# Kernel tuning notes

Measured on AMD Instinct MI355X. Metric: run time of the kernel, lower is better.

Reference implementation:

```python
import jax, jax.numpy as jnp
import numpy as np

N_NODES = 50000
N_EDGES = 800000
N_GRAPHS = 256


def setup_inputs() -> dict:
    key = jax.random.key(0)
    ks = jax.random.split(key, 20)
    s = 0.05
    return {
        "x": jax.random.normal(ks[0], (N_NODES, 128), jnp.float32),
        "edge_index": jax.random.randint(ks[1], (2, N_EDGES), 0, N_NODES, jnp.int64),
        "batch_index": jnp.sort(jax.random.randint(ks[2], (N_NODES,), 0, N_GRAPHS, jnp.int64)),
        "mol_features": jax.random.normal(ks[3], (N_GRAPHS, 256), jnp.float32),
        "gcn_W": jax.random.normal(ks[4], (3, 128, 128), jnp.float32) * s,
        "gcn_b": jax.random.normal(ks[5], (3, 128), jnp.float32) * s,
        "gcn_out_W": jax.random.normal(ks[6], (128, 128), jnp.float32) * s,
        "gcn_out_b": jax.random.normal(ks[7], (128,), jnp.float32) * s,
        "mlp_W": jax.random.normal(ks[8], (2, 256, 256), jnp.float32) * s,
        "mlp_b": jax.random.normal(ks[9], (2, 256), jnp.float32) * s,
        "mlp_out_W": jax.random.normal(ks[10], (64, 256), jnp.float32) * s,
        "mlp_out_b": jax.random.normal(ks[11], (64,), jnp.float32) * s,
        "pred_W1": jax.random.normal(ks[12], (256, 192), jnp.float32) * s,
        "pred_b1": jax.random.normal(ks[13], (256,), jnp.float32) * s,
        "pred_W2": jax.random.normal(ks[14], (256, 256), jnp.float32) * s,
        "pred_b2": jax.random.normal(ks[15], (256,), jnp.float32) * s,
        "out_W": jax.random.normal(ks[16], (1, 256), jnp.float32) * s,
        "out_b": jax.random.normal(ks[17], (1,), jnp.float32) * s,
    }


def reference(x, edge_index, batch_index, mol_features,
              gcn_W, gcn_b, gcn_out_W, gcn_out_b,
              mlp_W, mlp_b, mlp_out_W, mlp_out_b,
              pred_W1, pred_b1, pred_W2, pred_b2, out_W, out_b):
    N = x.shape[0]
    E = edge_index.shape[1]
    G = mol_features.shape[0]
    row, col = edge_index[0], edge_index[1]

    # GCN normalization with self-loops (PyG gcn_norm, symmetric):
    # deg[i] = in-degree(i) + 1 (self loop); norm_e = d^-1/2[row] * d^-1/2[col]
    deg = jax.ops.segment_sum(jnp.ones((E,), x.dtype), col, num_segments=N) + 1.0
    dinv = jax.lax.rsqrt(deg)
    enorm = (dinv[row] * dinv[col])[:, None]     # [E,1]
    self_c = (dinv * dinv)[:, None]              # [N,1] self-loop coefficient

    h1 = x
    for i in range(gcn_W.shape[0]):
        h = h1 @ gcn_W[i].T                      # per-node transform [N,128]
        agg = jax.ops.segment_sum(h[row] * enorm, col, num_segments=N)
        h1 = jax.nn.relu(agg + self_c * h + gcn_b[i])
    h1 = h1 @ gcn_out_W.T + gcn_out_b            # final GCN-branch Linear (no relu)

    # global_mean_pool over batch_index -> [G,128]
    sums = jax.ops.segment_sum(h1, batch_index, num_segments=G)
    counts = jax.ops.segment_sum(jnp.ones((N,), x.dtype), batch_index, num_segments=G)
    h1 = sums / jnp.maximum(counts, 1.0)[:, None]

    # MLP branch: relu after every linear (including last)
    h2 = mol_features
    for i in range(mlp_W.shape[0]):
        h2 = jax.nn.relu(h2 @ mlp_W[i].T + mlp_b[i])
    h2 = jax.nn.relu(h2 @ mlp_out_W.T + mlp_out_b)

    h = jnp.concatenate([h1, h2], axis=1)        # [G,192]
    h = jax.nn.relu(h @ pred_W1.T + pred_b1)
    h = jax.nn.relu(h @ pred_W2.T + pred_b2)
    return h @ out_W.T + out_b                   # [G,1]
```

## Files before the change

kernel.cpp:

```cpp
#include <hip/hip_runtime.h>


typedef __attribute__((ext_vector_type(8))) short short8;
typedef __attribute__((ext_vector_type(4))) float f32x4;

#define BKT 64
#define SL 16
#define CAP 192
#define WCAP 2560
#define NBINBLK 2048
#define HROWS 65536

__device__ __forceinline__ unsigned short f2bf(float f) {
    union { float f; unsigned u; } c; c.f = f;
    unsigned u = c.u;
    unsigned r = u + 0x7FFFu + ((u >> 16) & 1u);
    return (unsigned short)(r >> 16);
}
__device__ __forceinline__ float bflo(unsigned w) {
    union { unsigned u; float f; } c; c.u = w << 16; return c.f;
}
__device__ __forceinline__ float bfhi(unsigned w) {
    union { unsigned u; float f; } c; c.u = w & 0xFFFF0000u; return c.f;
}

__global__ void k_init(int* cur, float* pool, float* cnt,
                       const float* __restrict__ gcnW, uint4* __restrict__ Wb,
                       int M, int G) {
    int i = blockIdx.x * 256 + threadIdx.x;
    if (i < M * 16) cur[i] = 0;
    if (i < G * 128) pool[i] = 0.f;
    if (i < G) cnt[i] = 0.f;
    if (i < 3 * 2048) {
        int l = i >> 11, rem = i & 2047;
        int o = rem >> 4, c = rem & 15;
        const float4* s = (const float4*)(gcnW + (size_t)l * 16384 + o * 128 + c * 8);
        float4 a = s[0], b = s[1];
        uint4 v;
        v.x = ((unsigned)f2bf(a.y) << 16) | f2bf(a.x);
        v.y = ((unsigned)f2bf(a.w) << 16) | f2bf(a.z);
        v.z = ((unsigned)f2bf(b.y) << 16) | f2bf(b.x);
        v.w = ((unsigned)f2bf(b.w) << 16) | f2bf(b.z);
        Wb[(l << 11) | (o << 4) | (c ^ (o & 15))] = v;
    }
}

__global__ __launch_bounds__(256) void k_bin(const int* __restrict__ row,
                                             const int* __restrict__ col,
                                             int* __restrict__ cur,
                                             unsigned* __restrict__ gbin,
                                             int E, int C) {
    const int x = blockIdx.x & (SL - 1);
    int e0 = blockIdx.x * C, e1 = min(E, e0 + C);
    for (int e = e0 + threadIdx.x; e < e1; e += 256) {
        int c = col[e];
        int cell = (c >> 6) * SL + x;
        int cnt = atomicAdd(&cur[cell << 4], 1);
        gbin[cell * CAP + cnt] = (unsigned)row[e] | ((unsigned)(c & 63) << 16);
    }
}

__global__ __launch_bounds__(256) void k_csr(const unsigned* __restrict__ gbin,
                                             const int* __restrict__ cur,
                                             int* __restrict__ rs,
                                             unsigned short* __restrict__ rd,
                                             float* __restrict__ dinv,
                                             unsigned short* __restrict__ csrf,
                                             const float* __restrict__ x,
                                             unsigned short* __restrict__ xb,
                                             int N) {
    const int b = blockIdx.x, t = threadIdx.x;
    __shared__ int hcnt[64], lcur[64], fills[SL];
    __shared__ float sdinv[64];
    if (t < 64) hcnt[t] = 0;
    if (t < SL) fills[t] = cur[(b * SL + t) << 4];
    __syncthreads();
    #pragma unroll 4
    for (int xx = 0; xx < SL; ++xx) {
        int cbase = (b * SL + xx) * CAP, fill = fills[xx];
        for (int i = t; i < fill; i += 256)
            atomicAdd(&hcnt[(gbin[cbase + i] >> 16) & 63], 1);
    }
    __syncthreads();
    if (t < 64) {
        int v = hcnt[t], xs = v;
        #pragma unroll
        for (int off = 1; off < 64; off <<= 1) {
            int u = __shfl_up(xs, off, 64);
            if (t >= off) xs += u;
        }
        int excl = xs - v;
        lcur[t] = excl;
        float d = rsqrtf((float)v + 1.0f);
        sdinv[t] = d;
        int node = b * 64 + t;
        rs[node] = b * WCAP + excl;
        rd[node] = (unsigned short)v;
        dinv[node] = d;
    }
    __syncthreads();
    #pragma unroll 4
    for (int xx = 0; xx < SL; ++xx) {
        int cbase = (b * SL + xx) * CAP, fill = fills[xx];
        for (int i = t; i < fill; i += 256) {
            unsigned v = gbin[cbase + i];
            int p = atomicAdd(&lcur[(v >> 16) & 63], 1);
            csrf[b * WCAP + p] = (unsigned short)(v & 0xFFFFu);
        }
    }
    const int node0 = b * 64;
    #pragma unroll
    for (int it = 0; it < 4; ++it) {
        int i = t + it * 256;
        int nd = node0 + (i >> 4);
        if (nd < N) {
            int ch = i & 15;
            float d = sdinv[i >> 4];
            const float4* s = (const float4*)(x + (size_t)nd * 128 + ch * 8);
            float4 a = s[0], bb = s[1];
            uint4 o;
            o.x = ((unsigned)f2bf(d * a.y) << 16) | f2bf(d * a.x);
            o.y = ((unsigned)f2bf(d * a.w) << 16) | f2bf(d * a.z);
            o.z = ((unsigned)f2bf(d * bb.y) << 16) | f2bf(d * bb.x);
            o.w = ((unsigned)f2bf(d * bb.w) << 16) | f2bf(d * bb.z);
            *(uint4*)(xb + (size_t)nd * 128 + ch * 8) = o;
        }
    }
}

__global__ __launch_bounds__(256) void k_agg(const unsigned short* __restrict__ h,
                                             unsigned short* __restrict__ y,
                                             const float* __restrict__ dinv,
                                             const int* __restrict__ rs,
                                             const unsigned short* __restrict__ rd,
                                             const unsigned short* __restrict__ csrf,
                                             int N) {
    const int lane = threadIdx.x & 63;
    const int n = blockIdx.x * 4 + (threadIdx.x >> 6);
    if (n >= N) return;
    const int fg = lane & 15;
    const int slot = lane >> 4;
    const int s = rs[n], e = s + rd[n];

    float acc[8] = {0.f, 0.f, 0.f, 0.f, 0.f, 0.f, 0.f, 0.f};
    for (int base = s; base < e; base += 16) {
        int src_l = csrf[base + fg];
        #pragma unroll
        for (int i = 0; i < 4; ++i) {
            int j = i * 4 + slot;
            int src = __shfl(src_l, j, 16);
            uint4 v = *(const uint4*)(h + (size_t)src * 128 + fg * 8);
            bool ok = (base + j) < e;
            v.x = ok ? v.x : 0u; v.y = ok ? v.y : 0u;
            v.z = ok ? v.z : 0u; v.w = ok ? v.w : 0u;
            acc[0] += bflo(v.x); acc[1] += bfhi(v.x);
            acc[2] += bflo(v.y); acc[3] += bfhi(v.y);
            acc[4] += bflo(v.z); acc[5] += bfhi(v.z);
            acc[6] += bflo(v.w); acc[7] += bfhi(v.w);
        }
    }
    #pragma unroll
    for (int r = 0; r < 8; ++r) {
        acc[r] += __shfl_xor(acc[r], 16, 64);
        acc[r] += __shfl_xor(acc[r], 32, 64);
    }
    if (slot == 0) {
        float dn = dinv[n];
        uint4 hv = *(const uint4*)(h + (size_t)n * 128 + fg * 8);
        float sv[8] = {bflo(hv.x), bfhi(hv.x), bflo(hv.y), bfhi(hv.y),
                       bflo(hv.z), bfhi(hv.z), bflo(hv.w), bfhi(hv.w)};
        unsigned short ob[8];
        #pragma unroll
        for (int r = 0; r < 8; ++r) ob[r] = f2bf(dn * (acc[r] + sv[r]));
        uint4 o;
        o.x = ((unsigned)ob[1] << 16) | ob[0];
        o.y = ((unsigned)ob[3] << 16) | ob[2];
        o.z = ((unsigned)ob[5] << 16) | ob[4];
        o.w = ((unsigned)ob[7] << 16) | ob[6];
        *(uint4*)(y + (size_t)n * 128 + fg * 8) = o;
    }
}

__global__ __launch_bounds__(256) void k_mm(const unsigned short* __restrict__ A,
                                            const uint4* __restrict__ Wb,
                                            const float* __restrict__ bias,
                                            const float* __restrict__ dscale,
                                            unsigned short* __restrict__ C, int N) {
    __shared__ uint4 Wsh[2048];
    const int tid = threadIdx.x;
    #pragma unroll
    for (int it = 0; it < 8; ++it)
        Wsh[tid + it * 256] = Wb[tid + it * 256];

    const int lane = tid & 63;
    const int wv = tid >> 6;
    const int l15 = lane & 15, quad = lane >> 4;
    const int arow_i = blockIdx.x * 64 + wv * 16 + l15;
    const unsigned short* arow = A + (size_t)min(arow_i, N - 1) * 128;

    f32x4 acc[8];
    #pragma unroll
    for (int ct = 0; ct < 8; ++ct) acc[ct] = (f32x4){0.f, 0.f, 0.f, 0.f};

    __syncthreads();
    #pragma unroll
    for (int kiter = 0; kiter < 4; ++kiter) {
        short8 af = *(const short8*)(arow + kiter * 32 + quad * 8);
        const int cswz = (kiter * 4 + quad) ^ l15;
        #pragma unroll
        for (int ct = 0; ct < 8; ++ct) {
            short8 bf = *(const short8*)(&Wsh[((ct * 16 + l15) << 4) | cswz]);
            acc[ct] = __builtin_amdgcn_mfma_f32_16x16x32_bf16(af, bf, acc[ct], 0, 0, 0);
        }
    }

    const int rbase = blockIdx.x * 64 + wv * 16 + quad * 4;
    float ds[4];
    #pragma unroll
    for (int r = 0; r < 4; ++r) {
        int rr = rbase + r;
        ds[r] = (dscale && rr < N) ? dscale[rr] : 1.f;
    }
    #pragma unroll
    for (int ct = 0; ct < 8; ++ct) {
        int colc = ct * 16 + l15;
        float bcol = bias[colc];
        #pragma unroll
        for (int r = 0; r < 4; ++r) {
            int rr = rbase + r;
            if (rr < N) {
                float v = fmaxf(acc[ct][r] + bcol, 0.f) * ds[r];
                C[(size_t)rr * 128 + colc] = f2bf(v);
            }
        }
    }
}

__global__ __launch_bounds__(256) void k_pool(const unsigned short* __restrict__ h,
                                              const int* __restrict__ batch,
                                              float* __restrict__ pool,
                                              float* __restrict__ cnt, int N) {
    int t = threadIdx.x;
    int fg = t & 15, sg = t >> 4;
    int n0 = blockIdx.x * 512 + sg * 32;
    if (n0 >= N) return;
    int n1 = min(n0 + 32, N);
    int gprev = batch[n0];
    float racc[8] = {0.f, 0.f, 0.f, 0.f, 0.f, 0.f, 0.f, 0.f};
    float rcnt = 0.f;
    for (int n = n0; n < n1; ++n) {
        int g = batch[n];
        if (g != gprev) {
            float* dst = pool + (size_t)gprev * 128 + fg * 8;
            #pragma unroll
            for (int r = 0; r < 8; ++r) atomicAdd(dst + r, racc[r]);
            if (fg == 0) atomicAdd(&cnt[gprev], rcnt);
            #pragma unroll
            for (int r = 0; r < 8; ++r) racc[r] = 0.f;
            rcnt = 0.f; gprev = g;
        }
        uint4 v = *(const uint4*)(h + (size_t)n * 128 + fg * 8);
        racc[0] += bflo(v.x); racc[1] += bfhi(v.x);
        racc[2] += bflo(v.y); racc[3] += bfhi(v.y);
        racc[4] += bflo(v.z); racc[5] += bfhi(v.z);
        racc[6] += bflo(v.w); racc[7] += bfhi(v.w);
        rcnt += 1.f;
    }
    float* dst = pool + (size_t)gprev * 128 + fg * 8;
    #pragma unroll
    for (int r = 0; r < 8; ++r) atomicAdd(dst + r, racc[r]);
    if (fg == 0) atomicAdd(&cnt[gprev], rcnt);
}

__device__ __forceinline__ float dot8(const float* __restrict__ S,
                                      const float* __restrict__ w, int K32) {
    float a[8] = {0.f, 0.f, 0.f, 0.f, 0.f, 0.f, 0.f, 0.f};
    for (int i = 0; i < K32; ++i) {
        #pragma unroll
        for (int j = 0; j < 8; ++j) {
            float4 wv = *(const float4*)(w + i * 32 + j * 4);
            float4 sv = *(const float4*)(S + i * 32 + j * 4);
            a[j] += wv.x * sv.x + wv.y * sv.y + wv.z * sv.z + wv.w * sv.w;
        }
    }
    return ((a[0] + a[1]) + (a[2] + a[3])) + ((a[4] + a[5]) + (a[6] + a[7]));
}

__global__ __launch_bounds__(256) void k_head(
    const float* __restrict__ pool, const float* __restrict__ cnt,
    const float* __restrict__ gcnoW, const float* __restrict__ gcnob,
    const float* __restrict__ mol,
    const float* __restrict__ mlpW, const float* __restrict__ mlpb,
    const float* __restrict__ mloW, const float* __restrict__ mlob,
    const float* __restrict__ pW1, const float* __restrict__ pb1,
    const float* __restrict__ pW2, const float* __restrict__ pb2,
    const float* __restrict__ oW, const float* __restrict__ ob,
    float* __restrict__ out, int G) {
    const int g = blockIdx.x;
    const int t = threadIdx.x;
    __shared__ float A[256], B[256], Cc[192], Mn[128];
    __shared__ float red[4];

    A[t] = mol[(size_t)g * 256 + t];
    if (t < 128) {
        float c = cnt[g];
        Mn[t] = pool[(size_t)g * 128 + t] / fmaxf(c, 1.f);
    }
    __syncthreads();

    float v = dot8(A, mlpW + (size_t)t * 256, 8);
    B[t] = fmaxf(v + mlpb[t], 0.f);
    __syncthreads();

    v = dot8(B, mlpW + 65536 + (size_t)t * 256, 8);
    A[t] = fmaxf(v + mlpb[256 + t], 0.f);
    __syncthreads();

    if (t < 64) {
        float a2 = dot8(A, mloW + (size_t)t * 256, 8);
        Cc[128 + t] = fmaxf(a2 + mlob[t], 0.f);
    } else if (t < 192) {
        int o = t - 64;
        float a2 = dot8(Mn, gcnoW + (size_t)o * 128, 4);
        Cc[o] = a2 + gcnob[o];
    }
    __syncthreads();

    v = dot8(Cc, pW1 + (size_t)t * 192, 6);
    B[t] = fmaxf(v + pb1[t], 0.f);
    __syncthreads();

    v = dot8(B, pW2 + (size_t)t * 256, 8);
    float r = fmaxf(v + pb2[t], 0.f) * oW[t];
    #pragma unroll
    for (int off = 32; off > 0; off >>= 1) r += __shfl_xor(r, off, 64);
    if ((t & 63) == 0) red[t >> 6] = r;
    __syncthreads();
    if (t == 0) out[g] = red[0] + red[1] + red[2] + red[3] + ob[0];
}

extern "C" void kernel_launch(void* const* d_in, const int* in_sizes, int n_in,
                              void* d_out, int out_size, void* d_ws, size_t ws_size,
                              hipStream_t stream) {
    const float* x     = (const float*)d_in[0];
    const int*   ei    = (const int*)d_in[1];
    const int*   batch = (const int*)d_in[2];
    const float* mol   = (const float*)d_in[3];
    const float* gcnW  = (const float*)d_in[4];
    const float* gcnb  = (const float*)d_in[5];
    const float* gcnoW = (const float*)d_in[6];
    const float* gcnob = (const float*)d_in[7];
    const float* mlpW  = (const float*)d_in[8];
    const float* mlpb  = (const float*)d_in[9];
    const float* mloW  = (const float*)d_in[10];
    const float* mlob  = (const float*)d_in[11];
    const float* pW1   = (const float*)d_in[12];
    const float* pb1   = (const float*)d_in[13];
    const float* pW2   = (const float*)d_in[14];
    const float* pb2   = (const float*)d_in[15];
    const float* oW    = (const float*)d_in[16];
    const float* ob    = (const float*)d_in[17];

    const int N = in_sizes[0] / 128;
    const int E = in_sizes[1] / 2;
    const int G = in_sizes[3] / 256;
    const int* row = ei;
    const int* col = ei + E;

    const int NBK = (N + BKT - 1) / BKT;
    const int M = NBK * SL;
    const int C = (E + NBINBLK - 1) / NBINBLK;

    char* p = (char*)d_ws;
    auto alloc = [&](size_t bytes) {
        char* q = p;
        p += (bytes + 255) & ~(size_t)255;
        return (void*)q;
    };
    int*    rs    = (int*)alloc((size_t)NBK * 64 * 4);
    unsigned short* rd = (unsigned short*)alloc((size_t)NBK * 64 * 2);
    float*  dinv  = (float*)alloc((size_t)NBK * 64 * 4);
    int*    cur   = (int*)alloc((size_t)M * 16 * 4);
    unsigned* gbin = (unsigned*)alloc((size_t)M * CAP * 4);
    unsigned short* csrf = (unsigned short*)alloc(((size_t)NBK * WCAP + 32) * 2);
    unsigned short* xb   = (unsigned short*)alloc((size_t)HROWS * 128 * 2);
    unsigned short* bufA = (unsigned short*)alloc((size_t)HROWS * 128 * 2);
    unsigned short* bufB = (unsigned short*)alloc((size_t)HROWS * 128 * 2);
    uint4*  Wb    = (uint4*)alloc((size_t)3 * 2048 * 16);
    float*  pool  = (float*)alloc((size_t)G * 128 * 4);
    float*  cnt   = (float*)alloc((size_t)G * 4);

    const int initblocks = (M * 16 + 255) / 256;

    k_init<<<initblocks, 256, 0, stream>>>(cur, pool, cnt, gcnW, Wb, M, G);
    k_bin<<<NBINBLK, 256, 0, stream>>>(row, col, cur, gbin, E, C);
    k_csr<<<NBK, 256, 0, stream>>>(gbin, cur, rs, rd, dinv, csrf, x, xb, N);

    const int mmblocks = (N + 63) / 64;
    const int aggblocks = (N + 3) / 4;
    const unsigned short* src = xb;
    for (int l = 0; l < 3; ++l) {
        k_agg<<<aggblocks, 256, 0, stream>>>(src, bufA, dinv, rs, rd, csrf, N);
        k_mm<<<mmblocks, 256, 0, stream>>>(bufA, Wb + (size_t)l * 2048,
                                           gcnb + (size_t)l * 128,
                                           (l < 2) ? dinv : (const float*)nullptr,
                                           bufB, N);
        src = bufB;
    }
    k_pool<<<(N + 511) / 512, 256, 0, stream>>>(bufB, batch, pool, cnt, N);
    k_head<<<G, 256, 0, stream>>>(pool, cnt, gcnoW, gcnob, mol, mlpW, mlpb,
                                  mloW, mlob, pW1, pb1, pW2, pb2, oW, ob,
                                  (float*)d_out, G);
}
```

Before: 358.3 us.

## Batch 16 graphs per head block and use bf16 MFMA with pre-converted weights

The head MLP now processes 16 graphs per block and computes each linear layer with 16x16x32 bf16 MFMA tiles instead of per-thread fp32 dot products. The head weights are converted once to bf16 in the init kernel, so each block reads half the bytes and the weights are shared across 16 graphs instead of being reloaded per graph. The trade-off is far fewer blocks in flight (16 instead of 256) and reduced precision for activations and weights.

```diff
diff --git a/kernel.cpp b/kernel.cpp
--- a/kernel.cpp
+++ b/kernel.cpp
@@ -11,6 +11,14 @@
 #define NBINBLK 2048
 #define HROWS 65536
 
+#define HW_MLP0 0
+#define HW_MLP1 65536
+#define HW_MLO  131072
+#define HW_GCNO 147456
+#define HW_PW1  163840
+#define HW_PW2  212992
+#define HW_TOT  278528
+
 __device__ __forceinline__ unsigned short f2bf(float f) {
     union { float f; unsigned u; } c; c.f = f;
     unsigned u = c.u;
@@ -26,6 +34,9 @@
 
 __global__ void k_init(int* cur, float* pool, float* cnt,
                        const float* __restrict__ gcnW, uint4* __restrict__ Wb,
+                       const float* __restrict__ mlpW, const float* __restrict__ mloW,
+                       const float* __restrict__ gcnoW, const float* __restrict__ pW1,
+                       const float* __restrict__ pW2, unsigned short* __restrict__ Wh,
                        int M, int G) {
     int i = blockIdx.x * 256 + threadIdx.x;
     if (i < M * 16) cur[i] = 0;
@@ -43,6 +54,24 @@
         v.w = ((unsigned)f2bf(b.w) << 16) | f2bf(b.z);
         Wb[(l << 11) | (o << 4) | (c ^ (o & 15))] = v;
     }
+    int j = i - 8192;
+    if (j >= 0 && j < (HW_TOT / 8)) {
+        int e = j * 8;
+        const float* src;
+        if (e < HW_MLO)        src = mlpW  + e;
+        else if (e < HW_GCNO)  src = mloW  + (e - HW_MLO);
+        else if (e < HW_PW1)   src = gcnoW + (e - HW_GCNO);
+        else if (e < HW_PW2)   src = pW1   + (e - HW_PW1);
+        else                   src = pW2   + (e - HW_PW2);
+        float4 a = *(const float4*)src;
+        float4 b = *((const float4*)src + 1);
+        uint4 v;
+        v.x = ((unsigned)f2bf(a.y) << 16) | f2bf(a.x);
+        v.y = ((unsigned)f2bf(a.w) << 16) | f2bf(a.z);
+        v.z = ((unsigned)f2bf(b.y) << 16) | f2bf(b.x);
+        v.w = ((unsigned)f2bf(b.w) << 16) | f2bf(b.z);
+        *(uint4*)(Wh + e) = v;
+    }
 }
 
 __global__ __launch_bounds__(256) void k_bin(const int* __restrict__ row,
@@ -272,71 +301,116 @@
     if (fg == 0) atomicAdd(&cnt[gprev], rcnt);
 }
 
-__device__ __forceinline__ float dot8(const float* __restrict__ S,
-                                      const float* __restrict__ w, int K32) {
-    float a[8] = {0.f, 0.f, 0.f, 0.f, 0.f, 0.f, 0.f, 0.f};
-    for (int i = 0; i < K32; ++i) {
-        #pragma unroll
-        for (int j = 0; j < 8; ++j) {
-            float4 wv = *(const float4*)(w + i * 32 + j * 4);
-            float4 sv = *(const float4*)(S + i * 32 + j * 4);
-            a[j] += wv.x * sv.x + wv.y * sv.y + wv.z * sv.z + wv.w * sv.w;
-        }
-    }
-    return ((a[0] + a[1]) + (a[2] + a[3])) + ((a[4] + a[5]) + (a[6] + a[7]));
-}
-
 __global__ __launch_bounds__(256) void k_head(
+    const unsigned short* __restrict__ Wh,
     const float* __restrict__ pool, const float* __restrict__ cnt,
-    const float* __restrict__ gcnoW, const float* __restrict__ gcnob,
     const float* __restrict__ mol,
-    const float* __restrict__ mlpW, const float* __restrict__ mlpb,
-    const float* __restrict__ mloW, const float* __restrict__ mlob,
-    const float* __restrict__ pW1, const float* __restrict__ pb1,
-    const float* __restrict__ pW2, const float* __restrict__ pb2,
+    const float* __restrict__ mlpb, const float* __restrict__ mlob,
+    const float* __restrict__ gcnob,
+    const float* __restrict__ pb1, const float* __restrict__ pb2,
     const float* __restrict__ oW, const float* __restrict__ ob,
     float* __restrict__ out, int G) {
-    const int g = blockIdx.x;
+    const int g0 = blockIdx.x * 16;
     const int t = threadIdx.x;
-    __shared__ float A[256], B[256], Cc[192], Mn[128];
-    __shared__ float red[4];
-
-    A[t] = mol[(size_t)g * 256 + t];
-    if (t < 128) {
-        float c = cnt[g];
-        Mn[t] = pool[(size_t)g * 128 + t] / fmaxf(c, 1.f);
-    }
-    __syncthreads();
-
-    float v = dot8(A, mlpW + (size_t)t * 256, 8);
-    B[t] = fmaxf(v + mlpb[t], 0.f);
-    __syncthreads();
-
-    v = dot8(B, mlpW + 65536 + (size_t)t * 256, 8);
-    A[t] = fmaxf(v + mlpb[256 + t], 0.f);
-    __syncthreads();
-
-    if (t < 64) {
-        float a2 = dot8(A, mloW + (size_t)t * 256, 8);
-        Cc[128 + t] = fmaxf(a2 + mlob[t], 0.f);
-    } else if (t < 192) {
-        int o = t - 64;
-        float a2 = dot8(Mn, gcnoW + (size_t)o * 128, 4);
-        Cc[o] = a2 + gcnob[o];
-    }
-    __syncthreads();
-
-    v = dot8(Cc, pW1 + (size_t)t * 192, 6);
-    B[t] = fmaxf(v + pb1[t], 0.f);
-    __syncthreads();
-
-    v = dot8(B, pW2 + (size_t)t * 256, 8);
-    float r = fmaxf(v + pb2[t], 0.f) * oW[t];
-    #pragma unroll
-    for (int off = 32; off > 0; off >>= 1) r += __shfl_xor(r, off, 64);
-    if ((t & 63) == 0) red[t >> 6] = r;
-    __syncthreads();
-    if (t == 0) out[g] = red[0] + red[1] + red[2] + red[3] + ob[0];
+    const int lane = t & 63, wv = t >> 6;
+    const int l15 = lane & 15, quad = lane >> 4;
+    __shared__ unsigned short A[16][264], B[16][264], Cc[16][200], Mn[16][136];
+    __shared__ float red[4][16];
+
+    for (int i = t; i < 16 * 256; i += 256) {
+        int g = i >> 8, k = i & 255;
+        A[g][k] = f2bf(mol[(size_t)(g0 + g) * 256 + k]);
+    }
+    for (int i = t; i < 16 * 128; i += 256) {
+        int g = i >> 7, k = i & 127;
+        float c = cnt[g0 + g];
+        Mn[g][k] = f2bf(pool[(size_t)(g0 + g) * 128 + k] / fmaxf(c, 1.f));
+    }
+    __syncthreads();
+
+    auto do_tile = [&](const unsigned short* actb, int astr, int K,
+                       const unsigned short* W, int orow,
+                       const float* __restrict__ bias, int bidx,
+                       unsigned short* dstb, int dstr, int ocol, bool dorelu) {
+        f32x4 c = {0.f, 0.f, 0.f, 0.f};
+        for (int kt = 0; kt < (K >> 5); ++kt) {
+            short8 af = *(const short8*)(actb + (size_t)l15 * astr + kt * 32 + quad * 8);
+            short8 bf = *(const short8*)(W + (size_t)orow * K + kt * 32 + quad * 8);
+            c = __builtin_amdgcn_mfma_f32_16x16x32_bf16(af, bf, c, 0, 0, 0);
+        }
+        float bb = bias[bidx];
+        #pragma unroll
+        for (int r = 0; r < 4; ++r) {
+            int g = quad * 4 + r;
+            float v = c[r] + bb;
+            if (dorelu) v = fmaxf(v, 0.f);
+            dstb[(size_t)g * dstr + ocol] = f2bf(v);
+        }
+    };
+
+    #pragma unroll
+    for (int nt = 0; nt < 4; ++nt) {
+        int o = (wv * 4 + nt) * 16 + l15;
+        do_tile(&A[0][0], 264, 256, Wh + HW_MLP0, o, mlpb, o, &B[0][0], 264, o, true);
+    }
+    __syncthreads();
+    #pragma unroll
+    for (int nt = 0; nt < 4; ++nt) {
+        int o = (wv * 4 + nt) * 16 + l15;
+        do_tile(&B[0][0], 264, 256, Wh + HW_MLP1, o, mlpb + 256, o, &A[0][0], 264, o, true);
+    }
+    __syncthreads();
+    #pragma unroll
+    for (int j = 0; j < 3; ++j) {
+        int tile = wv * 3 + j;
+        if (tile < 8) {
+            int o = tile * 16 + l15;
+            do_tile(&Mn[0][0], 136, 128, Wh + HW_GCNO, o, gcnob, o, &Cc[0][0], 200, o, false);
+        } else {
+            int om = (tile - 8) * 16 + l15;
+            do_tile(&A[0][0], 264, 256, Wh + HW_MLO, om, mlob, om, &Cc[0][0], 200, 128 + om, true);
+        }
+    }
+    __syncthreads();
+    #pragma unroll
+    for (int nt = 0; nt < 4; ++nt) {
+        int o = (wv * 4 + nt) * 16 + l15;
+        do_tile(&Cc[0][0], 200, 192, Wh + HW_PW1, o, pb1, o, &B[0][0], 264, o, true);
+    }
+    __syncthreads();
+    {
+        float pacc[4] = {0.f, 0.f, 0.f, 0.f};
+        #pragma unroll
+        for (int nt = 0; nt < 4; ++nt) {
+            int o = (wv * 4 + nt) * 16 + l15;
+            f32x4 c = {0.f, 0.f, 0.f, 0.f};
+            #pragma unroll
+            for (int kt = 0; kt < 8; ++kt) {
+                short8 af = *(const short8*)(&B[0][0] + (size_t)l15 * 264 + kt * 32 + quad * 8);
+                short8 bf = *(const short8*)(Wh + HW_PW2 + (size_t)o * 256 + kt * 32 + quad * 8);
+                c = __builtin_amdgcn_mfma_f32_16x16x32_bf16(af, bf, c, 0, 0, 0);
+            }
+            float bb = pb2[o], wo = oW[o];
+            #pragma unroll
+            for (int r = 0; r < 4; ++r)
+                pacc[r] += fmaxf(c[r] + bb, 0.f) * wo;
+        }
+        #pragma unroll
+        for (int off = 1; off < 16; off <<= 1)
+            #pragma unroll
+            for (int r = 0; r < 4; ++r)
+                pacc[r] += __shfl_xor(pacc[r], off, 64);
+        if (l15 == 0) {
+            #pragma unroll
+            for (int r = 0; r < 4; ++r)
+                red[wv][quad * 4 + r] = pacc[r];
+        }
+    }
+    __syncthreads();
+    if (t < 16) {
+        float s = red[0][t] + red[1][t] + red[2][t] + red[3][t] + ob[0];
+        if (g0 + t < G) out[g0 + t] = s;
+    }
 }
 
 extern "C" void kernel_launch(void* const* d_in, const int* in_sizes, int n_in,
@@ -387,12 +461,14 @@
     unsigned short* bufA = (unsigned short*)alloc((size_t)HROWS * 128 * 2);
     unsigned short* bufB = (unsigned short*)alloc((size_t)HROWS * 128 * 2);
     uint4*  Wb    = (uint4*)alloc((size_t)3 * 2048 * 16);
+    unsigned short* Wh = (unsigned short*)alloc((size_t)HW_TOT * 2);
     float*  pool  = (float*)alloc((size_t)G * 128 * 4);
     float*  cnt   = (float*)alloc((size_t)G * 4);
 
     const int initblocks = (M * 16 + 255) / 256;
 
-    k_init<<<initblocks, 256, 0, stream>>>(cur, pool, cnt, gcnW, Wb, M, G);
+    k_init<<<initblocks, 256, 0, stream>>>(cur, pool, cnt, gcnW, Wb,
+                                           mlpW, mloW, gcnoW, pW1, pW2, Wh, M, G);
     k_bin<<<NBINBLK, 256, 0, stream>>>(row, col, cur, gbin, E, C);
     k_csr<<<NBK, 256, 0, stream>>>(gbin, cur, rs, rd, dinv, csrf, x, xb, N);
 
@@ -408,7 +484,7 @@
         src = bufB;
     }
     k_pool<<<(N + 511) / 512, 256, 0, stream>>>(bufB, batch, pool, cnt, N);
-    k_head<<<G, 256, 0, stream>>>(pool, cnt, gcnoW, gcnob, mol, mlpW, mlpb,
-                                  mloW, mlob, pW1, pb1, pW2, pb2, oW, ob,
-                                  (float*)d_out, G);
-}
+    k_head<<<(G + 15) / 16, 256, 0, stream>>>(
+        Wh, pool, cnt, mol, mlpb, mlob, gcnob, pb1, pb2, oW, ob,
+        (float*)d_out, G);
+}
```

Measured after the change: 349.4 us. 2.5% less time.
